# Kernel tuning notes

Hardware: AMD Instinct MI355X
Metric: run time of the kernel (lower is better)

Reference implementation:

```python
import jax, jax.numpy as jnp
import numpy as np
from jax import lax

B, CIN, H, W = 2, 512, 64, 64
CD = CIN // 2            # down_dim = 256
CQ = CD // 8             # q/k channels = 32
EPS = 1e-5               # BatchNorm eps


def _conv3(x, w, b):
    # 3x3 conv, stride 1, padding 1 (init padding=1), NCHW/OIHW
    y = lax.conv_general_dilated(x, w, (1, 1), [(1, 1), (1, 1)],
                                 dimension_numbers=('NCHW', 'OIHW', 'NCHW'))
    return y + b[None, :, None, None]


def _bn(x, g, b, m, v):
    scale = g / jnp.sqrt(v + EPS)
    return x * scale[None, :, None, None] + (b - m * scale)[None, :, None, None]


def _prelu(x, a):
    return jnp.where(x > 0, x, a * x)


def _p1(x, w, b):
    # 1x1 conv as channel matmul
    return jnp.einsum('bchw,oc->bohw', x, w) + b[None, :, None, None]


def setup_inputs() -> dict:
    key = jax.random.key(0)
    it = iter(jax.random.split(key, 64))
    def nrm(shape, s=0.05):
        return jax.random.normal(next(it), shape, jnp.float32) * s
    inp = {
        'input_rgb': jax.random.normal(next(it), (B, CIN, H, W), jnp.float32),
        'input_dsm': jax.random.normal(next(it), (B, CIN, H, W), jnp.float32),
    }
    for m in ('rgb', 'dsm'):
        inp['conv_w_' + m] = nrm((CD, CIN, 3, 3))
        inp['conv_b_' + m] = nrm((CD,))
        inp['bn_g_' + m] = 1.0 + nrm((CD,))
        inp['bn_b_' + m] = nrm((CD,))
        inp['bn_m_' + m] = nrm((CD,))
        inp['bn_v_' + m] = jax.random.uniform(next(it), (CD,), jnp.float32, 0.5, 1.5)
        inp['prelu_' + m] = jnp.float32(0.25)
        inp['q_w_' + m] = nrm((CQ, CD)); inp['q_b_' + m] = nrm((CQ,))
        inp['k_w_' + m] = nrm((CQ, CD)); inp['k_b_' + m] = nrm((CQ,))
        inp['v_w_' + m] = nrm((CD, CD)); inp['v_b_' + m] = nrm((CD,))
        inp['up_w_' + m] = nrm((CIN, CD)); inp['up_b_' + m] = nrm((CIN,))
        inp['gamma_' + m] = jnp.float32(0.1)  # learned residual gate (zero-init in torch)
    return inp


def reference(input_rgb, input_dsm,
              conv_w_rgb, conv_b_rgb, bn_g_rgb, bn_b_rgb, bn_m_rgb, bn_v_rgb, prelu_rgb,
              q_w_rgb, q_b_rgb, k_w_rgb, k_b_rgb, v_w_rgb, v_b_rgb, up_w_rgb, up_b_rgb, gamma_rgb,
              conv_w_dsm, conv_b_dsm, bn_g_dsm, bn_b_dsm, bn_m_dsm, bn_v_dsm, prelu_dsm,
              q_w_dsm, q_b_dsm, k_w_dsm, k_b_dsm, v_w_dsm, v_b_dsm, up_w_dsm, up_b_dsm, gamma_dsm):
    conv_rgb = _prelu(_bn(_conv3(input_rgb, conv_w_rgb, conv_b_rgb),
                          bn_g_rgb, bn_b_rgb, bn_m_rgb, bn_v_rgb), prelu_rgb)
    conv_dsm = _prelu(_bn(_conv3(input_dsm, conv_w_dsm, conv_b_dsm),
                          bn_g_dsm, bn_b_dsm, bn_m_dsm, bn_v_dsm), prelu_dsm)
    b, c, h, w = conv_rgb.shape
    n = h * w
    q_rgb = _p1(conv_rgb, q_w_rgb, q_b_rgb).reshape(b, CQ, n)
    k_rgb = _p1(conv_rgb, k_w_rgb, k_b_rgb).reshape(b, CQ, n)
    v_rgb = _p1(conv_rgb, v_w_rgb, v_b_rgb).reshape(b, c, n)
    q_dsm = _p1(conv_dsm, q_w_dsm, q_b_dsm).reshape(b, CQ, n)
    k_dsm = _p1(conv_dsm, k_w_dsm, k_b_dsm).reshape(b, CQ, n)
    v_dsm = _p1(conv_dsm, v_w_dsm, v_b_dsm).reshape(b, c, n)
    # cross-modal unscaled attention: dsm queries attend over rgb keys
    attn_rgb = jax.nn.softmax(jnp.einsum('bqn,bqm->bnm', q_dsm, k_rgb), axis=-1)  # [b,n,n]
    o_rgb = jnp.einsum('bcj,bij->bci', v_rgb, attn_rgb).reshape(b, c, h, w)
    o_rgb = gamma_rgb * o_rgb + conv_rgb
    attn_dsm = jax.nn.softmax(jnp.einsum('bqn,bqm->bnm', q_rgb, k_dsm), axis=-1)
    o_dsm = jnp.einsum('bcj,bij->bci', v_dsm, attn_dsm).reshape(b, c, h, w)
    o_dsm = gamma_dsm * o_dsm + conv_dsm
    out_rgb = _p1(o_rgb, up_w_rgb, up_b_rgb) + input_rgb
    out_dsm = _p1(o_dsm, up_w_dsm, up_b_dsm) + input_dsm
    return (out_rgb, out_dsm)
```

## Files before the change

### kernel.cpp

```cpp
#include <hip/hip_runtime.h>
#include <hip/hip_bf16.h>
#include <stdint.h>


constexpr int CINCH = 512;
constexpr int NPIX  = 4096;

typedef __bf16 bf16x8 __attribute__((ext_vector_type(8)));
typedef __bf16 bf16x4 __attribute__((ext_vector_type(4)));
typedef float  f32x4  __attribute__((ext_vector_type(4)));

__device__ __forceinline__ __bf16 f2b(float f) {
    __hip_bfloat16 h = __float2bfloat16(f);
    return *reinterpret_cast<__bf16*>(&h);
}

__device__ __forceinline__ void load_lds16(const void* g, void* l) {
    __builtin_amdgcn_global_load_lds(
        (const __attribute__((address_space(1))) unsigned int*)(uintptr_t)g,
        (__attribute__((address_space(3))) unsigned int*)(uintptr_t)l,
        16, 0, 0);
}

__global__ __launch_bounds__(256)
void prep_w(const float* __restrict__ w_r, const float* __restrict__ w_d,
            const float* __restrict__ cb_r, const float* __restrict__ bg_r,
            const float* __restrict__ bb_r, const float* __restrict__ bm_r,
            const float* __restrict__ bv_r,
            const float* __restrict__ cb_d, const float* __restrict__ bg_d,
            const float* __restrict__ bb_d, const float* __restrict__ bm_d,
            const float* __restrict__ bv_d,
            __bf16* __restrict__ Wt, float* __restrict__ scA,
            float* __restrict__ shB, __bf16* __restrict__ zrow)
{
    const int t = threadIdx.x;
    const int blk = blockIdx.x;
    if (blk < 2304) {
        int gid = blk * 1024 + t * 4;
        int mod = gid >= 1179648;
        int o2  = gid - mod * 1179648;
        int tap = o2 >> 17;
        int r   = o2 & 131071;
        int oc  = r >> 9;
        int ic  = r & 511;
        const float* wsrc = mod ? w_d : w_r;
        long base = ((long)(oc * 512 + ic)) * 9 + tap;
        bf16x4 v;
        v.x = f2b(wsrc[base]);
        v.y = f2b(wsrc[base + 9]);
        v.z = f2b(wsrc[base + 18]);
        v.w = f2b(wsrc[base + 27]);
        *(bf16x4*)&Wt[gid] = v;
    } else if (blk == 2304) {
        unsigned short* z = (unsigned short*)zrow;
        z[t] = 0; z[t + 256] = 0;
    } else {
        int mod = blk - 2305;
        const float* cb = mod ? cb_d : cb_r;
        const float* bg = mod ? bg_d : bg_r;
        const float* bb = mod ? bb_d : bb_r;
        const float* bm = mod ? bm_d : bm_r;
        const float* bv = mod ? bv_d : bv_r;
        int oc = t;
        float sc = bg[oc] * rsqrtf(bv[oc] + 1e-5f);
        scA[mod * 256 + oc] = sc;
        shB[mod * 256 + oc] = (cb[oc] - bm[oc]) * sc + bb[oc];
    }
}

__global__ __launch_bounds__(256)
void prep_gw(const float* __restrict__ qw_r, const float* __restrict__ qw_d,
             const float* __restrict__ kw_r, const float* __restrict__ kw_d,
             const float* __restrict__ vw_r, const float* __restrict__ vw_d,
             const float* __restrict__ uw_r, const float* __restrict__ uw_d,
             __bf16* __restrict__ Wq, __bf16* __restrict__ Wk,
             __bf16* __restrict__ Wv, __bf16* __restrict__ Wu)
{
    int gid = blockIdx.x * 1024 + threadIdx.x * 4;
    __bf16* dst;
    float4 f = make_float4(0.f, 0.f, 0.f, 0.f);
    if (gid < 65536) {
        int mod = gid >> 15, e = gid & 32767;
        dst = Wq + gid;
        if (e < 8192) f = *(const float4*)((mod ? qw_d : qw_r) + e);
    } else if (gid < 131072) {
        int g = gid - 65536;
        int mod = g >> 15, e = g & 32767;
        dst = Wk + g;
        if (e < 8192) f = *(const float4*)((mod ? kw_d : kw_r) + e);
    } else if (gid < 262144) {
        int g = gid - 131072;
        int mod = g >> 16, e = g & 65535;
        dst = Wv + g;
        f = *(const float4*)((mod ? vw_d : vw_r) + e);
    } else {
        int g = gid - 262144;
        int mod = g >> 17, e = g & 131071;
        dst = Wu + g;
        f = *(const float4*)((mod ? uw_d : uw_r) + e);
    }
    bf16x4 o; o.x = f2b(f.x); o.y = f2b(f.y); o.z = f2b(f.z); o.w = f2b(f.w);
    *(bf16x4*)dst = o;
}

__global__ __launch_bounds__(256)
void xpose(const float* __restrict__ inr, const float* __restrict__ ind,
           __bf16* __restrict__ Xp)
{
    __shared__ float tile[32][33];
    const int t = threadIdx.x;
    const int p0 = blockIdx.x * 32;
    const int ic0 = blockIdx.y * 32;
    const int mb = blockIdx.z;
    const int mod = mb >> 1, b = mb & 1;
    const float* src = (mod ? ind : inr) + (long)b * CINCH * NPIX;

    int i = t >> 3, j4 = (t & 7) * 4;
    float4 v = *(const float4*)&src[(long)(ic0 + i) * NPIX + p0 + j4];
    tile[i][j4 + 0] = v.x; tile[i][j4 + 1] = v.y;
    tile[i][j4 + 2] = v.z; tile[i][j4 + 3] = v.w;
    __syncthreads();
    int j = t >> 3, i4 = (t & 7) * 4;
    bf16x4 o;
    o.x = f2b(tile[i4 + 0][j]);
    o.y = f2b(tile[i4 + 1][j]);
    o.z = f2b(tile[i4 + 2][j]);
    o.w = f2b(tile[i4 + 3][j]);
    *(bf16x4*)&Xp[((long)mb * NPIX + p0 + j) * 512 + ic0 + i4] = o;
}

__global__ __launch_bounds__(256)
void t256(const float* __restrict__ src, __bf16* __restrict__ dst)
{
    __shared__ float tile[32][33];
    const int t = threadIdx.x;
    const int p0 = blockIdx.x * 32;
    const int c0 = blockIdx.y * 32;
    const int mb = blockIdx.z;
    const float* s = src + (long)mb * 256 * NPIX;
    __bf16* d = dst + (long)mb * NPIX * 256;

    int i = t >> 3, j4 = (t & 7) * 4;
    float4 v = *(const float4*)&s[(long)(c0 + i) * NPIX + p0 + j4];
    tile[i][j4 + 0] = v.x; tile[i][j4 + 1] = v.y;
    tile[i][j4 + 2] = v.z; tile[i][j4 + 3] = v.w;
    __syncthreads();
    int j = t >> 3, i4 = (t & 7) * 4;
    bf16x4 o;
    o.x = f2b(tile[i4 + 0][j]); o.y = f2b(tile[i4 + 1][j]);
    o.z = f2b(tile[i4 + 2][j]); o.w = f2b(tile[i4 + 3][j]);
    *(bf16x4*)&d[((long)(p0 + j)) * 256 + c0 + i4] = o;
}

__global__ __launch_bounds__(256)
void conv_mfma(const __bf16* __restrict__ Wt, const __bf16* __restrict__ Xp,
               const __bf16* __restrict__ zrow, const float* __restrict__ scA,
               const float* __restrict__ shB, const float* __restrict__ prr,
               const float* __restrict__ prd, float* __restrict__ conv)
{
    __shared__ __bf16 As[3 * 64 * 64];
    __shared__ __bf16 Bs[2 * 385 * 64];

    const int t = threadIdx.x;
    const int y0 = blockIdx.x * 4;
    const int m0 = blockIdx.y * 64;
    const int mb = blockIdx.z;
    const int mod = mb >> 1;

    const __bf16* Am = Wt + (long)mod * (9 * 256 * 512);
    const __bf16* Xb = Xp + (long)mb * NPIX * 512;

    const int lane = t & 63, quad = lane >> 4, l15 = lane & 15, w = t >> 6;

    if (t < 16)
        *(f32x4*)((char*)Bs + (t >> 3) * 49280 + 49152 + (t & 7) * 16) = (f32x4)0.f;
    asm volatile("s_waitcnt lgkmcnt(0)" ::: "memory");

    auto stage_a = [&](int buf, int tap, int cc) {
#pragma unroll
        for (int k = 0; k < 2; ++k) {
            int r  = w * 16 + k * 8 + (lane >> 3);
            int sl = (lane & 7) ^ (r & 7);
            const __bf16* src = Am + (long)tap * 131072 + (long)(m0 + r) * 512
                              + cc * 64 + sl * 8;
            load_lds16(src, (char*)As + buf * 8192 + (w * 16 + k * 8) * 128);
        }
    };
    auto stage_b = [&](int buf, int cc) {
#pragma unroll
        for (int k = 0; k < 12; ++k) {
            int r  = w * 96 + k * 8 + (lane >> 3);
            int sl = (lane & 7) ^ (r & 7);
            int hr = r >> 6, xx = r & 63;
            int gy = y0 + hr - 1;
            const __bf16* src = ((unsigned)gy < 64u)
                ? Xb + (long)(gy * 64 + xx) * 512 + cc * 64 + sl * 8
                : zrow + sl * 8;
            load_lds16(src, (char*)Bs + buf * 49280 + (w * 96 + k * 8) * 128);
        }
    };

    f32x4 acc[4][4];
#pragma unroll
    for (int i = 0; i < 4; ++i)
#pragma unroll
        for (int j = 0; j < 4; ++j) acc[i][j] = (f32x4)0.f;

    stage_b(0, 0);
    stage_a(0, 0, 0);
    stage_a(1, 1, 0);

    const int soffA0 = ((quad ^ (l15 & 7)) << 4);
    const int soffA1 = (((4 | quad) ^ (l15 & 7)) << 4);

    for (int c = 0; c < 8; ++c) {
        for (int tp = 0; tp < 9; ++tp) {
            const int s = c * 9 + tp;
            if (s == 71)                  { asm volatile("s_waitcnt vmcnt(0)" ::: "memory"); }
            else if (tp >= 7 && c < 7)    { asm volatile("s_waitcnt vmcnt(14)" ::: "memory"); }
            else                          { asm volatile("s_waitcnt vmcnt(2)" ::: "memory"); }
            __builtin_amdgcn_sched_barrier(0);
            __builtin_amdgcn_s_barrier();
            __builtin_amdgcn_sched_barrier(0);

            if (s + 2 < 72) {
                int c2 = (tp + 2 >= 9) ? c + 1 : c;
                int t2 = (tp + 2 >= 9) ? tp - 7 : tp + 2;
                int b2 = (s + 2) % 3;
                stage_a(b2, t2, c2);
            }
            __builtin_amdgcn_sched_barrier(0);
            if (tp == 6 && c < 7) stage_b((c + 1) & 1, c + 1);
            __builtin_amdgcn_sched_barrier(0);

            const char* ab = (const char*)As + (s % 3) * 8192;
            const char* bb = (const char*)Bs + (c & 1) * 49280;
            const int dy = tp / 3 - 1, dx = tp % 3 - 1;
            const int hr = w + 1 + dy;
            int rb[4];
#pragma unroll
            for (int fj = 0; fj < 4; ++fj) {
                int x = fj * 16 + l15 + dx;
                rb[fj] = ((unsigned)x < 64u) ? hr * 64 + x : 384;
            }
#pragma unroll
            for (int kk = 0; kk < 2; ++kk) {
                const int slq = kk * 4 + quad;
                bf16x8 af[4], bfr[4];
#pragma unroll
                for (int i = 0; i < 4; ++i)
                    af[i] = *(const bf16x8*)(ab + (16 * i + l15) * 128
                                             + (kk ? soffA1 : soffA0));
#pragma unroll
                for (int fj = 0; fj < 4; ++fj)
                    bfr[fj] = *(const bf16x8*)(bb + rb[fj] * 128
                                               + ((slq ^ (rb[fj] & 7)) << 4));
#pragma unroll
                for (int i = 0; i < 4; ++i)
#pragma unroll
                    for (int fj = 0; fj < 4; ++fj)
                        acc[i][fj] = __builtin_amdgcn_mfma_f32_16x16x32_bf16(
                            af[i], bfr[fj], acc[i][fj], 0, 0, 0);
            }
        }
    }

    const float alpha = (mod ? prd : prr)[0];
    float* outp = conv + (long)mb * 256 * NPIX;
    const int nbase = (y0 + w) * 64;
#pragma unroll
    for (int i = 0; i < 4; ++i) {
#pragma unroll
        for (int r = 0; r < 4; ++r) {
            int oc = m0 + 16 * i + quad * 4 + r;
            float sc = scA[mod * 256 + oc];
            float sh = shB[mod * 256 + oc];
            float* orow = outp + (long)oc * NPIX;
#pragma unroll
            for (int fj = 0; fj < 4; ++fj) {
                int n = nbase + 16 * fj + l15;
                float y = acc[i][fj][r] * sc + sh;
                y = (y > 0.f) ? y : alpha * y;
                orow[n] = y;
            }
        }
    }
}

__global__ __launch_bounds__(256)
void proj_mfma(const __bf16* __restrict__ Wb, int mstride,
               const __bf16* __restrict__ Bt,
               const float* __restrict__ bias_r, const float* __restrict__ bias_d,
               __bf16* __restrict__ dstT, __bf16* __restrict__ dstV,
               float* __restrict__ dstU,
               const float* __restrict__ resid_r, const float* __restrict__ resid_d,
               int mode, float oscale)
{
    __shared__ __bf16 As[128 * 32];
    __shared__ __bf16 Bs[128 * 32];

    const int t = threadIdx.x;
    const int n0 = blockIdx.x * 128;
    const int m0 = blockIdx.y * 128;
    const int mb = blockIdx.z;
    const int mod = mb >> 1, b = mb & 1;

    const __bf16* Am = Wb + (long)mod * mstride;
    const __bf16* Bm = Bt + (long)mb * (NPIX * 256);
    const float* bias = mod ? bias_d : bias_r;

    const int rowa = t >> 2, c16 = t & 3;
    char* ldsA0 = (char*)As + (t >> 6) * 1024;
    char* ldsA1 = ldsA0 + 4096;
    char* ldsB0 = (char*)Bs + (t >> 6) * 1024;
    char* ldsB1 = ldsB0 + 4096;
    const __bf16* srcA = Am + (long)(m0 + rowa) * 256 + c16 * 8;
    const __bf16* srcB = Bm + (long)(n0 + rowa) * 256 + c16 * 8;

    const int lane = t & 63, quad = lane >> 4, l15 = lane & 15, w = t >> 6;
    const int mw = (w >> 1) * 64, nw = (w & 1) * 64;
    const char* abase = (const char*)As + (mw + l15) * 64 + quad * 16;
    const char* bbase = (const char*)Bs + (nw + l15) * 64 + quad * 16;

    f32x4 acc[4][4];
#pragma unroll
    for (int i = 0; i < 4; ++i)
#pragma unroll
        for (int j = 0; j < 4; ++j) acc[i][j] = (f32x4)0.f;

    for (int kc = 0; kc < 256; kc += 32) {
        load_lds16(srcA + kc, ldsA0);
        load_lds16(srcA + kc + 16384, ldsA1);
        load_lds16(srcB + kc, ldsB0);
        load_lds16(srcB + kc + 16384, ldsB1);
        __syncthreads();

        bf16x8 af[4], bfr[4];
#pragma unroll
        for (int i = 0; i < 4; ++i) af[i]  = *(const bf16x8*)(abase + i * 1024);
#pragma unroll
        for (int j = 0; j < 4; ++j) bfr[j] = *(const bf16x8*)(bbase + j * 1024);
#pragma unroll
        for (int i = 0; i < 4; ++i)
#pragma unroll
            for (int j = 0; j < 4; ++j)
                acc[i][j] = __builtin_amdgcn_mfma_f32_16x16x32_bf16(
                    af[i], bfr[j], acc[i][j], 0, 0, 0);
        __syncthreads();
    }

    if (mode == 0) {
        if (mw == 0) {
            __bf16* dbase = dstT + (long)mb * (NPIX * 32);
#pragma unroll
            for (int fi = 0; fi < 2; ++fi)
#pragma unroll
                for (int r = 0; r < 4; ++r) {
                    int oc = 16 * fi + quad * 4 + r;
                    float bi = bias[oc];
#pragma unroll
                    for (int fj = 0; fj < 4; ++fj) {
                        int n = n0 + nw + 16 * fj + l15;
                        dbase[(long)n * 32 + oc] = f2b((acc[fi][fj][r] + bi) * oscale);
                    }
                }
        }
    } else if (mode == 1) {
        __bf16* dv = dstV + (long)mb * (256 * NPIX);
#pragma unroll
        for (int fi = 0; fi < 4; ++fi)
#pragma unroll
            for (int r = 0; r < 4; ++r) {
                int c = m0 + mw + 16 * fi + quad * 4 + r;
                float bi = bias[c];
                __bf16* row = dv + (long)c * NPIX;
#pragma unroll
                for (int fj = 0; fj < 4; ++fj) {
                    int n = n0 + nw + 16 * fj + l15;
                    row[n] = f2b(acc[fi][fj][r] + bi);
                }
            }
    } else {
        float* du = dstU + (long)mod * 4194304 + (long)b * 2097152;
        const float* rs = (mod ? resid_d : resid_r) + (long)b * 2097152;
#pragma unroll
        for (int fi = 0; fi < 4; ++fi)
#pragma unroll
            for (int r = 0; r < 4; ++r) {
                int oc = m0 + mw + 16 * fi + quad * 4 + r;
                float bi = bias[oc];
                const float* rrow = rs + (long)oc * NPIX;
                float* orow = du + (long)oc * NPIX;
#pragma unroll
                for (int fj = 0; fj < 4; ++fj) {
                    int n = n0 + nw + 16 * fj + l15;
                    orow[n] = acc[fi][fj][r] + bi + rrow[n];
                }
            }
    }
}

__global__ __launch_bounds__(256)
void attn_stats_mfma(const __bf16* __restrict__ Qt, const __bf16* __restrict__ Kt,
                     float* __restrict__ rmp, float* __restrict__ rlp)
{
    __shared__ __bf16 Qs[128 * 32];
    __shared__ __bf16 Ks[128 * 32];
    __shared__ float redm[2][128];
    __shared__ float redl[2][128];

    const int t  = threadIdx.x;
    const int i0 = blockIdx.x * 128;
    const int mbo = blockIdx.y;
    const int o  = mbo >> 1, b = mbo & 1;
    const int seg = blockIdx.z;
    const int jbase = seg * 1024;
    const int mbK = o * 2 + b, mbQ = (1 - o) * 2 + b;

    const __bf16* Qg = Qt + (long)mbQ * 131072;
    const __bf16* Kg = Kt + (long)mbK * 131072;

    const int lane = t & 63, quad = lane >> 4, l15 = lane & 15, w = t >> 6;
    const int mS = (w >> 1) * 64;
    const int nS = (w & 1) * 64;

    load_lds16((const char*)Qg + (long)i0 * 64 + t * 16, (char*)Qs + w * 1024);
    load_lds16((const char*)Qg + (long)i0 * 64 + 4096 + t * 16,
               (char*)Qs + 4096 + w * 1024);
    __syncthreads();

    bf16x8 qa[4];
#pragma unroll
    for (int fi = 0; fi < 4; ++fi)
        qa[fi] = *(const bf16x8*)((const char*)Qs + (mS + 16 * fi + l15) * 64 + quad * 16);

    const f32x4 zero4 = (f32x4)0.f;
    float m_t[16], l_t[16];
#pragma unroll
    for (int e = 0; e < 16; ++e) { m_t[e] = -3.0e38f; l_t[e] = 0.f; }

    for (int j0 = jbase; j0 < jbase + 1024; j0 += 128) {
        __syncthreads();
        load_lds16((const char*)Kg + (long)j0 * 64 + t * 16, (char*)Ks + w * 1024);
        load_lds16((const char*)Kg + (long)j0 * 64 + 4096 + t * 16,
                   (char*)Ks + 4096 + w * 1024);
        __syncthreads();

        bf16x8 kb[4];
#pragma unroll
        for (int fj = 0; fj < 4; ++fj)
            kb[fj] = *(const bf16x8*)((const char*)Ks + (nS + 16 * fj + l15) * 64 + quad * 16);
#pragma unroll
        for (int fi = 0; fi < 4; ++fi) {
            f32x4 sf[4];
#pragma unroll
            for (int fj = 0; fj < 4; ++fj)
                sf[fj] = __builtin_amdgcn_mfma_f32_16x16x32_bf16(qa[fi], kb[fj], zero4, 0, 0, 0);
#pragma unroll
            for (int r = 0; r < 4; ++r) {
                int e = fi * 4 + r;
                float a = fmaxf(fmaxf(sf[0][r], sf[1][r]), fmaxf(sf[2][r], sf[3][r]));
                float nm = fmaxf(m_t[e], a);
                float s = exp2f(sf[0][r] - nm) + exp2f(sf[1][r] - nm)
                        + exp2f(sf[2][r] - nm) + exp2f(sf[3][r] - nm);
                l_t[e] = l_t[e] * exp2f(m_t[e] - nm) + s;
                m_t[e] = nm;
            }
        }
    }

#pragma unroll
    for (int d = 1; d < 16; d <<= 1)
#pragma unroll
        for (int e = 0; e < 16; ++e) {
            float om = __shfl_xor(m_t[e], d, 64);
            float ol = __shfl_xor(l_t[e], d, 64);
            float nm = fmaxf(m_t[e], om);
            l_t[e] = l_t[e] * exp2f(m_t[e] - nm) + ol * exp2f(om - nm);
            m_t[e] = nm;
        }
    if (l15 == 0) {
#pragma unroll
        for (int fi = 0; fi < 4; ++fi)
#pragma unroll
            for (int r = 0; r < 4; ++r) {
                redm[w & 1][mS + 16 * fi + quad * 4 + r] = m_t[fi * 4 + r];
                redl[w & 1][mS + 16 * fi + quad * 4 + r] = l_t[fi * 4 + r];
            }
    }
    __syncthreads();
    if (t < 128) {
        float m0 = redm[0][t], m1 = redm[1][t];
        float l0 = redl[0][t], l1 = redl[1][t];
        float m = fmaxf(m0, m1);
        float l = l0 * exp2f(m0 - m) + l1 * exp2f(m1 - m);
        rmp[seg * 16384 + mbo * 4096 + i0 + t] = m;
        rlp[seg * 16384 + mbo * 4096 + i0 + t] = l;
    }
}

__global__ __launch_bounds__(256)
void stats_merge(const float* __restrict__ rmp, const float* __restrict__ rlp,
                 float* __restrict__ rmb, float* __restrict__ rlb)
{
    int idx = blockIdx.x * 256 + threadIdx.x;
    float m = rmp[idx];
#pragma unroll
    for (int s = 1; s < 4; ++s) m = fmaxf(m, rmp[s * 16384 + idx]);
    float l = 0.f;
#pragma unroll
    for (int s = 0; s < 4; ++s)
        l += rlp[s * 16384 + idx] * exp2f(rmp[s * 16384 + idx] - m);
    rmb[idx] = m;
    rlb[idx] = 1.f / l;
}

__global__ __launch_bounds__(256)
void attn_pv_mfma(const __bf16* __restrict__ Qt, const __bf16* __restrict__ Kt,
                  const __bf16* __restrict__ Vb,
                  float* __restrict__ part0, float* __restrict__ part1,
                  const float* __restrict__ rmb, const float* __restrict__ rlb)
{
    __shared__ __bf16 Qs[64 * 32];
    __shared__ __bf16 Ks[64 * 32];
    __shared__ __bf16 Vs[2 * 256 * 32];
    __shared__ __bf16 Ps[64 * 64];

    const int t  = threadIdx.x;
    const int i0 = blockIdx.x * 64;
    const int seg = blockIdx.y;
    const int mb = blockIdx.z;
    const int o  = mb >> 1, b = mb & 1;
    const int mbK = mb, mbQ = (1 - o) * 2 + b;
    const int jbase = seg * 2048;

    const __bf16* Qg = Qt + (long)mbQ * 131072;
    const __bf16* Kg = Kt + (long)mbK * 131072;
    const __bf16* Vg = Vb + (long)mbK * 1048576;
    const float* rm = rmb + mb * 4096;
    const float* rl = rlb + mb * 4096;

    const int lane = t & 63, quad = lane >> 4, l15 = lane & 15, w = t >> 6;
    const int iS = w * 16;
    const int cw = w * 64;

    load_lds16((const char*)Qg + (long)i0 * 64 + t * 16, (char*)Qs + w * 1024);

    float mlv[4], rlv[4];
#pragma unroll
    for (int r = 0; r < 4; ++r) mlv[r] = rm[i0 + iS + quad * 4 + r];
#pragma unroll
    for (int fj = 0; fj < 4; ++fj) rlv[fj] = rl[i0 + 16 * fj + l15];

    f32x4 acc[4][4];
#pragma unroll
    for (int i = 0; i < 4; ++i)
#pragma unroll
        for (int j = 0; j < 4; ++j) acc[i][j] = (f32x4)0.f;
    const f32x4 zero4 = (f32x4)0.f;

    __syncthreads();
    const bf16x8 qa = *(const bf16x8*)((const char*)Qs + (iS + l15) * 64 + quad * 16);

    const int clv = w * 16 + (lane >> 2);
    const int jb8 = (lane & 3) * 8;

    for (int j0 = jbase; j0 < jbase + 2048; j0 += 64) {
        __syncthreads();
        load_lds16((const char*)Kg + (long)j0 * 64 + t * 16, (char*)Ks + w * 1024);
        __syncthreads();

#pragma unroll
        for (int ii = 0; ii < 8; ++ii) {
            int ks = ii >> 2;
            int c = (ii & 3) * 64 + clv;
            load_lds16((const char*)Vg + (long)c * 8192 + (long)(j0 + ks * 32 + jb8) * 2,
                       (char*)Vs + ii * 4096 + w * 1024);
        }

        f32x4 sA[4];
#pragma unroll
        for (int fj = 0; fj < 4; ++fj) {
            bf16x8 kb = *(const bf16x8*)((const char*)Ks + (16 * fj + l15) * 64 + quad * 16);
            sA[fj] = __builtin_amdgcn_mfma_f32_16x16x32_bf16(qa, kb, zero4, 0, 0, 0);
        }
#pragma unroll
        for (int fj = 0; fj < 4; ++fj)
#pragma unroll
            for (int r = 0; r < 4; ++r) {
                int il = iS + quad * 4 + r;
                int boff = (il * 128 + (16 * fj + l15) * 2) ^ ((il & 12) << 3);
                *(__bf16*)((char*)Ps + boff) = f2b(exp2f(sA[fj][r] - mlv[r]));
            }
        __syncthreads();

#pragma unroll
        for (int ks = 0; ks < 2; ++ks) {
            bf16x8 va[4], pb[4];
#pragma unroll
            for (int fi = 0; fi < 4; ++fi)
                va[fi] = *(const bf16x8*)((const char*)Vs + ks * 16384 +
                                          (cw + 16 * fi + l15) * 64 + quad * 16);
#pragma unroll
            for (int fj = 0; fj < 4; ++fj) {
                int ip = 16 * fj + l15;
                int boff = (ip * 128 + ks * 64 + quad * 16) ^ ((ip & 12) << 3);
                pb[fj] = *(const bf16x8*)((const char*)Ps + boff);
            }
#pragma unroll
            for (int fi = 0; fi < 4; ++fi)
#pragma unroll
                for (int fj = 0; fj < 4; ++fj)
                    acc[fi][fj] = __builtin_amdgcn_mfma_f32_16x16x32_bf16(
                        va[fi], pb[fj], acc[fi][fj], 0, 0, 0);
        }
    }

    float* pg = (seg ? part1 : part0) + (long)mb * 1048576;
#pragma unroll
    for (int fi = 0; fi < 4; ++fi) {
#pragma unroll
        for (int r = 0; r < 4; ++r) {
            int c = cw + 16 * fi + quad * 4 + r;
            float* zr = pg + (long)c * 4096;
#pragma unroll
            for (int fj = 0; fj < 4; ++fj)
                zr[i0 + 16 * fj + l15] = acc[fi][fj][r] * rlv[fj];
        }
    }
}

__global__ __launch_bounds__(256)
void zred_t(const float* __restrict__ p0, const float* __restrict__ p1,
            const float* __restrict__ convb, __bf16* __restrict__ Zt,
            const float* __restrict__ g_r, const float* __restrict__ g_d)
{
    __shared__ float tile[32][33];
    const int t = threadIdx.x;
    const int pix0 = blockIdx.x * 32;
    const int c0 = blockIdx.y * 32;
    const int mb = blockIdx.z;
    const int o = mb >> 1;
    const float gamma = (o ? g_d : g_r)[0];
    const long base = (long)mb * 1048576;

    int i = t >> 3, j4 = (t & 7) * 4;
    long row = base + (long)(c0 + i) * 4096 + pix0 + j4;
    float4 a = *(const float4*)&p0[row];
    float4 b = *(const float4*)&p1[row];
    float4 cv = *(const float4*)&convb[row];
    tile[i][j4 + 0] = gamma * (a.x + b.x) + cv.x;
    tile[i][j4 + 1] = gamma * (a.y + b.y) + cv.y;
    tile[i][j4 + 2] = gamma * (a.z + b.z) + cv.z;
    tile[i][j4 + 3] = gamma * (a.w + b.w) + cv.w;
    __syncthreads();
    int j = t >> 3, i4 = (t & 7) * 4;
    bf16x4 oq;
    oq.x = f2b(tile[i4 + 0][j]); oq.y = f2b(tile[i4 + 1][j]);
    oq.z = f2b(tile[i4 + 2][j]); oq.w = f2b(tile[i4 + 3][j]);
    *(bf16x4*)&Zt[(long)mb * NPIX * 256 + (long)(pix0 + j) * 256 + c0 + i4] = oq;
}

extern "C" void kernel_launch(void* const* d_in, const int* in_sizes, int n_in,
                              void* d_out, int out_size, void* d_ws, size_t ws_size,
                              hipStream_t stream)
{
    const float* in_rgb = (const float*)d_in[0];
    const float* in_dsm = (const float*)d_in[1];
    auto P = [&](int i) { return (const float*)d_in[i]; };

    float* ws    = (float*)d_ws;
    float* conv  = ws;
    float* part0 = ws + 4194304;
    float* rmb   = ws + 8388608;
    float* rlb   = ws + 8404992;
    float* rmp   = part0;
    float* rlp   = part0 + 65536;
    float* scA   = ws + 8486912;
    float* shB   = ws + 8487424;
    __bf16* zrow = (__bf16*)(ws + 8487936);
    __bf16* Wt   = (__bf16*)(ws + 8488192);
    __bf16* Xp   = (__bf16*)(ws + 9667840);
    float*  part1 = ws + 9667840;
    __bf16* Qt   = (__bf16*)(ws + 13862144);
    __bf16* Kt   = (__bf16*)(ws + 14124288);
    __bf16* Vbb  = (__bf16*)(ws + 14386432);
    __bf16* Ct   = (__bf16*)(ws + 16483584);
    __bf16* Zt   = (__bf16*)(ws + 18580736);
    __bf16* Wq   = (__bf16*)(ws + 20677888);
    __bf16* Wk   = (__bf16*)(ws + 20710656);
    __bf16* Wv   = (__bf16*)(ws + 20743424);
    __bf16* Wu   = (__bf16*)(ws + 20808960);

    prep_w<<<2307, 256, 0, stream>>>(
        P(2), P(18), P(3), P(4), P(5), P(6), P(7),
        P(19), P(20), P(21), P(22), P(23),
        Wt, scA, shB, zrow);
    prep_gw<<<512, 256, 0, stream>>>(
        P(9), P(25), P(11), P(27), P(13), P(29), P(15), P(31),
        Wq, Wk, Wv, Wu);
    xpose<<<dim3(128, 16, 4), 256, 0, stream>>>(in_rgb, in_dsm, Xp);

    conv_mfma<<<dim3(16, 4, 4), 256, 0, stream>>>(
        Wt, Xp, zrow, scA, shB, P(8), P(24), conv);
    t256<<<dim3(128, 8, 4), 256, 0, stream>>>(conv, Ct);

    proj_mfma<<<dim3(32, 1, 4), 256, 0, stream>>>(
        Wq, 32768, Ct, P(10), P(26), Qt, nullptr, nullptr, nullptr, nullptr,
        0, 1.4426950408889634f);
    proj_mfma<<<dim3(32, 1, 4), 256, 0, stream>>>(
        Wk, 32768, Ct, P(12), P(28), Kt, nullptr, nullptr, nullptr, nullptr,
        0, 1.0f);
    proj_mfma<<<dim3(32, 2, 4), 256, 0, stream>>>(
        Wv, 65536, Ct, P(14), P(30), nullptr, Vbb, nullptr, nullptr, nullptr,
        1, 1.0f);

    attn_stats_mfma<<<dim3(32, 4, 4), 256, 0, stream>>>(Qt, Kt, rmp, rlp);
    stats_merge<<<64, 256, 0, stream>>>(rmp, rlp, rmb, rlb);

    attn_pv_mfma<<<dim3(64, 2, 4), 256, 0, stream>>>(
        Qt, Kt, Vbb, part0, part1, rmb, rlb);

    zred_t<<<dim3(128, 8, 4), 256, 0, stream>>>(
        part0, part1, conv, Zt, P(17), P(33));

    proj_mfma<<<dim3(32, 4, 4), 256, 0, stream>>>(
        Wu, 131072, Zt, P(16), P(32), nullptr, nullptr, (float*)d_out,
        in_rgb, in_dsm, 2, 1.0f);
}
```

Baseline: 367.0 us.

## Triple-buffer K/V loads, double P tile, and swizzle LDS in attention kernels

The PV attention kernel now handles 128 query rows per block instead of 64. K and V tiles are triple-buffered in LDS and the next stage is issued before computing the current one, with manual waitcnt and raw barriers in place of __syncthreads. The P tile is double-buffered, and both the stats and PV kernels use an XOR swizzle on global-to-LDS load offsets to reduce bank conflicts. The grid is flattened so that blocks sharing a K/V head are interleaved, aiming at L2 reuse. The cost is much larger LDS use and 128 accumulator registers, which forces one block per CU.

```diff
diff --git a/kernel.cpp b/kernel.cpp
--- a/kernel.cpp
+++ b/kernel.cpp
@@ -424,15 +424,19 @@
     const int mS = (w >> 1) * 64;
     const int nS = (w & 1) * 64;
 
-    load_lds16((const char*)Qg + (long)i0 * 64 + t * 16, (char*)Qs + w * 1024);
-    load_lds16((const char*)Qg + (long)i0 * 64 + 4096 + t * 16,
+    const int drow = w * 16 + (lane >> 2);
+    const int ssl  = ((lane & 3) ^ ((lane >> 3) & 3)) * 16;
+    const int rsl  = (quad ^ ((l15 >> 1) & 3)) << 4;
+
+    load_lds16((const char*)Qg + (long)(i0 + drow) * 64 + ssl, (char*)Qs + w * 1024);
+    load_lds16((const char*)Qg + (long)(i0 + 64 + drow) * 64 + ssl,
                (char*)Qs + 4096 + w * 1024);
     __syncthreads();
 
     bf16x8 qa[4];
 #pragma unroll
     for (int fi = 0; fi < 4; ++fi)
-        qa[fi] = *(const bf16x8*)((const char*)Qs + (mS + 16 * fi + l15) * 64 + quad * 16);
+        qa[fi] = *(const bf16x8*)((const char*)Qs + (mS + 16 * fi + l15) * 64 + rsl);
 
     const f32x4 zero4 = (f32x4)0.f;
     float m_t[16], l_t[16];
@@ -441,15 +445,15 @@
 
     for (int j0 = jbase; j0 < jbase + 1024; j0 += 128) {
         __syncthreads();
-        load_lds16((const char*)Kg + (long)j0 * 64 + t * 16, (char*)Ks + w * 1024);
-        load_lds16((const char*)Kg + (long)j0 * 64 + 4096 + t * 16,
+        load_lds16((const char*)Kg + (long)(j0 + drow) * 64 + ssl, (char*)Ks + w * 1024);
+        load_lds16((const char*)Kg + (long)(j0 + 64 + drow) * 64 + ssl,
                    (char*)Ks + 4096 + w * 1024);
         __syncthreads();
 
         bf16x8 kb[4];
 #pragma unroll
         for (int fj = 0; fj < 4; ++fj)
-            kb[fj] = *(const bf16x8*)((const char*)Ks + (nS + 16 * fj + l15) * 64 + quad * 16);
+            kb[fj] = *(const bf16x8*)((const char*)Ks + (nS + 16 * fj + l15) * 64 + rsl);
 #pragma unroll
         for (int fi = 0; fi < 4; ++fi) {
             f32x4 sf[4];
@@ -515,102 +519,136 @@
     rlb[idx] = 1.f / l;
 }
 
-__global__ __launch_bounds__(256)
+__global__ __launch_bounds__(256, 1)
 void attn_pv_mfma(const __bf16* __restrict__ Qt, const __bf16* __restrict__ Kt,
                   const __bf16* __restrict__ Vb,
                   float* __restrict__ part0, float* __restrict__ part1,
                   const float* __restrict__ rmb, const float* __restrict__ rlb)
 {
-    __shared__ __bf16 Qs[64 * 32];
-    __shared__ __bf16 Ks[64 * 32];
-    __shared__ __bf16 Vs[2 * 256 * 32];
-    __shared__ __bf16 Ps[64 * 64];
+    __shared__ __bf16 Qs[128 * 32];
+    __shared__ __bf16 Ks[3 * 64 * 32];
+    __shared__ __bf16 Vs[3 * 2 * 256 * 32];
+    __shared__ __bf16 Ps[2 * 128 * 64];
 
     const int t  = threadIdx.x;
-    const int i0 = blockIdx.x * 64;
-    const int seg = blockIdx.y;
-    const int mb = blockIdx.z;
+    const int bx = blockIdx.x;
+    const int grp = bx & 7;
+    const int i0  = (bx >> 3) * 128;
+    const int seg = grp & 1;
+    const int mb  = grp >> 1;
     const int o  = mb >> 1, b = mb & 1;
-    const int mbK = mb, mbQ = (1 - o) * 2 + b;
+    const int mbQ = (1 - o) * 2 + b;
     const int jbase = seg * 2048;
 
     const __bf16* Qg = Qt + (long)mbQ * 131072;
-    const __bf16* Kg = Kt + (long)mbK * 131072;
-    const __bf16* Vg = Vb + (long)mbK * 1048576;
+    const __bf16* Kg = Kt + (long)mb * 131072;
+    const __bf16* Vg = Vb + (long)mb * 1048576;
     const float* rm = rmb + mb * 4096;
     const float* rl = rlb + mb * 4096;
 
     const int lane = t & 63, quad = lane >> 4, l15 = lane & 15, w = t >> 6;
-    const int iS = w * 16;
+    const int iw = w * 32;
     const int cw = w * 64;
 
-    load_lds16((const char*)Qg + (long)i0 * 64 + t * 16, (char*)Qs + w * 1024);
-
-    float mlv[4], rlv[4];
-#pragma unroll
-    for (int r = 0; r < 4; ++r) mlv[r] = rm[i0 + iS + quad * 4 + r];
-#pragma unroll
-    for (int fj = 0; fj < 4; ++fj) rlv[fj] = rl[i0 + 16 * fj + l15];
-
-    f32x4 acc[4][4];
-#pragma unroll
-    for (int i = 0; i < 4; ++i)
-#pragma unroll
-        for (int j = 0; j < 4; ++j) acc[i][j] = (f32x4)0.f;
-    const f32x4 zero4 = (f32x4)0.f;
-
-    __syncthreads();
-    const bf16x8 qa = *(const bf16x8*)((const char*)Qs + (iS + l15) * 64 + quad * 16);
-
-    const int clv = w * 16 + (lane >> 2);
-    const int jb8 = (lane & 3) * 8;
-
-    for (int j0 = jbase; j0 < jbase + 2048; j0 += 64) {
-        __syncthreads();
-        load_lds16((const char*)Kg + (long)j0 * 64 + t * 16, (char*)Ks + w * 1024);
-        __syncthreads();
-
+    const int drow = w * 16 + (lane >> 2);
+    const int ssl  = ((lane & 3) ^ ((lane >> 3) & 3)) * 16;
+    const int rsl  = (quad ^ ((l15 >> 1) & 3)) << 4;
+
+    float mlv[8], rlv[8];
+#pragma unroll
+    for (int fi = 0; fi < 2; ++fi)
+#pragma unroll
+        for (int r = 0; r < 4; ++r)
+            mlv[fi * 4 + r] = rm[i0 + iw + 16 * fi + quad * 4 + r];
+#pragma unroll
+    for (int fj = 0; fj < 8; ++fj) rlv[fj] = rl[i0 + 16 * fj + l15];
+    asm volatile("s_waitcnt vmcnt(0)" ::: "memory");
+
+    load_lds16((const char*)Qg + (long)(i0 + drow) * 64 + ssl, (char*)Qs + w * 1024);
+    load_lds16((const char*)Qg + (long)(i0 + 64 + drow) * 64 + ssl,
+               (char*)Qs + 4096 + w * 1024);
+    asm volatile("s_waitcnt vmcnt(0)" ::: "memory");
+    __builtin_amdgcn_s_barrier();
+    bf16x8 qa[2];
+    qa[0] = *(const bf16x8*)((const char*)Qs + (iw + l15) * 64 + rsl);
+    qa[1] = *(const bf16x8*)((const char*)Qs + (iw + 16 + l15) * 64 + rsl);
+
+    auto stage = [&](int sidx) {
+        const int buf = sidx % 3;
+        const int j0 = jbase + sidx * 64;
+        load_lds16((const char*)Kg + (long)(j0 + drow) * 64 + ssl,
+                   (char*)Ks + buf * 4096 + w * 1024);
 #pragma unroll
         for (int ii = 0; ii < 8; ++ii) {
             int ks = ii >> 2;
-            int c = (ii & 3) * 64 + clv;
-            load_lds16((const char*)Vg + (long)c * 8192 + (long)(j0 + ks * 32 + jb8) * 2,
-                       (char*)Vs + ii * 4096 + w * 1024);
-        }
-
-        f32x4 sA[4];
+            int c  = (ii & 3) * 64 + drow;
+            load_lds16((const char*)Vg + (long)c * 8192 + (long)(j0 + ks * 32) * 2 + ssl,
+                       (char*)Vs + buf * 32768 + ii * 4096 + w * 1024);
+        }
+    };
+
+    f32x4 acc[4][8];
+#pragma unroll
+    for (int i = 0; i < 4; ++i)
+#pragma unroll
+        for (int j = 0; j < 8; ++j) acc[i][j] = (f32x4)0.f;
+    const f32x4 zero4 = (f32x4)0.f;
+
+    stage(0);
+
+    for (int s = 0; s < 32; ++s) {
+        if (s + 1 < 32) {
+            stage(s + 1);
+            asm volatile("s_waitcnt vmcnt(9)" ::: "memory");
+        } else {
+            asm volatile("s_waitcnt vmcnt(0)" ::: "memory");
+        }
+        __builtin_amdgcn_sched_barrier(0);
+        __builtin_amdgcn_s_barrier();
+        __builtin_amdgcn_sched_barrier(0);
+
+        const char* kbp = (const char*)Ks + (s % 3) * 4096;
+        f32x4 sA[2][4];
 #pragma unroll
         for (int fj = 0; fj < 4; ++fj) {
-            bf16x8 kb = *(const bf16x8*)((const char*)Ks + (16 * fj + l15) * 64 + quad * 16);
-            sA[fj] = __builtin_amdgcn_mfma_f32_16x16x32_bf16(qa, kb, zero4, 0, 0, 0);
-        }
-#pragma unroll
-        for (int fj = 0; fj < 4; ++fj)
-#pragma unroll
-            for (int r = 0; r < 4; ++r) {
-                int il = iS + quad * 4 + r;
-                int boff = (il * 128 + (16 * fj + l15) * 2) ^ ((il & 12) << 3);
-                *(__bf16*)((char*)Ps + boff) = f2b(exp2f(sA[fj][r] - mlv[r]));
-            }
-        __syncthreads();
-
+            bf16x8 kb = *(const bf16x8*)(kbp + (16 * fj + l15) * 64 + rsl);
+            sA[0][fj] = __builtin_amdgcn_mfma_f32_16x16x32_bf16(qa[0], kb, zero4, 0, 0, 0);
+            sA[1][fj] = __builtin_amdgcn_mfma_f32_16x16x32_bf16(qa[1], kb, zero4, 0, 0, 0);
+        }
+        char* pst = (char*)Ps + (s & 1) * 16384;
+#pragma unroll
+        for (int fi = 0; fi < 2; ++fi)
+#pragma unroll
+            for (int fj = 0; fj < 4; ++fj)
+#pragma unroll
+                for (int r = 0; r < 4; ++r) {
+                    int il = iw + 16 * fi + quad * 4 + r;
+                    int boff = (il * 128 + (16 * fj + l15) * 2) ^ ((il & 7) << 4);
+                    *(__bf16*)(pst + boff) = f2b(exp2f(sA[fi][fj][r] - mlv[fi * 4 + r]));
+                }
+        __builtin_amdgcn_sched_barrier(0);
+        __builtin_amdgcn_s_barrier();
+        __builtin_amdgcn_sched_barrier(0);
+
+        const char* vbp = (const char*)Vs + (s % 3) * 32768;
+        const char* prd = (const char*)Ps + (s & 1) * 16384;
 #pragma unroll
         for (int ks = 0; ks < 2; ++ks) {
-            bf16x8 va[4], pb[4];
+            bf16x8 va[4], pb[8];
 #pragma unroll
             for (int fi = 0; fi < 4; ++fi)
-                va[fi] = *(const bf16x8*)((const char*)Vs + ks * 16384 +
-                                          (cw + 16 * fi + l15) * 64 + quad * 16);
-#pragma unroll
-            for (int fj = 0; fj < 4; ++fj) {
+                va[fi] = *(const bf16x8*)(vbp + ks * 16384 +
+                                          (cw + 16 * fi + l15) * 64 + rsl);
+#pragma unroll
+            for (int fj = 0; fj < 8; ++fj) {
                 int ip = 16 * fj + l15;
-                int boff = (ip * 128 + ks * 64 + quad * 16) ^ ((ip & 12) << 3);
-                pb[fj] = *(const bf16x8*)((const char*)Ps + boff);
+                int boff = (ip * 128 + ks * 64 + quad * 16) ^ ((ip & 7) << 4);
+                pb[fj] = *(const bf16x8*)(prd + boff);
             }
 #pragma unroll
             for (int fi = 0; fi < 4; ++fi)
 #pragma unroll
-                for (int fj = 0; fj < 4; ++fj)
+                for (int fj = 0; fj < 8; ++fj)
                     acc[fi][fj] = __builtin_amdgcn_mfma_f32_16x16x32_bf16(
                         va[fi], pb[fj], acc[fi][fj], 0, 0, 0);
         }
@@ -624,7 +662,7 @@
             int c = cw + 16 * fi + quad * 4 + r;
             float* zr = pg + (long)c * 4096;
 #pragma unroll
-            for (int fj = 0; fj < 4; ++fj)
+            for (int fj = 0; fj < 8; ++fj)
                 zr[i0 + 16 * fj + l15] = acc[fi][fj][r] * rlv[fj];
         }
     }
@@ -718,7 +756,7 @@
     attn_stats_mfma<<<dim3(32, 4, 4), 256, 0, stream>>>(Qt, Kt, rmp, rlp);
     stats_merge<<<64, 256, 0, stream>>>(rmp, rlp, rmb, rlb);
 
-    attn_pv_mfma<<<dim3(64, 2, 4), 256, 0, stream>>>(
+    attn_pv_mfma<<<256, 256, 0, stream>>>(
         Qt, Kt, Vbb, part0, part1, rmb, rlb);
 
     zred_t<<<dim3(128, 8, 4), 256, 0, stream>>>(
```

Result: no change. 374.0 us (+1.9%).

## Swizzle LDS layouts for Q/K/V tiles and remap attention PV block order

Applied to the files above, without the earlier changes.

Changes the global-to-LDS load mapping for Q, K and V tiles in the attention stats and PV kernels to an XOR-swizzled layout, with matching swizzled reads, to reduce LDS bank conflicts on the MFMA operand loads. The Ps tile swizzle pattern is also changed. The PV kernel switches to a 1D grid where adjacent blocks share the same query tile across modality/segment, which may change cache locality. A launch-bounds occupancy hint of 2 blocks per SIMD set is added, which may constrain register allocation.

```diff
diff --git a/kernel.cpp b/kernel.cpp
--- a/kernel.cpp
+++ b/kernel.cpp
@@ -424,15 +424,19 @@
     const int mS = (w >> 1) * 64;
     const int nS = (w & 1) * 64;
 
-    load_lds16((const char*)Qg + (long)i0 * 64 + t * 16, (char*)Qs + w * 1024);
-    load_lds16((const char*)Qg + (long)i0 * 64 + 4096 + t * 16,
+    const int drow = w * 16 + (lane >> 2);
+    const int ssl  = ((lane & 3) ^ ((lane >> 3) & 3)) * 16;
+    const int rsl  = (quad ^ ((l15 >> 1) & 3)) << 4;
+
+    load_lds16((const char*)Qg + (long)(i0 + drow) * 64 + ssl, (char*)Qs + w * 1024);
+    load_lds16((const char*)Qg + (long)(i0 + 64 + drow) * 64 + ssl,
                (char*)Qs + 4096 + w * 1024);
     __syncthreads();
 
     bf16x8 qa[4];
 #pragma unroll
     for (int fi = 0; fi < 4; ++fi)
-        qa[fi] = *(const bf16x8*)((const char*)Qs + (mS + 16 * fi + l15) * 64 + quad * 16);
+        qa[fi] = *(const bf16x8*)((const char*)Qs + (mS + 16 * fi + l15) * 64 + rsl);
 
     const f32x4 zero4 = (f32x4)0.f;
     float m_t[16], l_t[16];
@@ -441,15 +445,15 @@
 
     for (int j0 = jbase; j0 < jbase + 1024; j0 += 128) {
         __syncthreads();
-        load_lds16((const char*)Kg + (long)j0 * 64 + t * 16, (char*)Ks + w * 1024);
-        load_lds16((const char*)Kg + (long)j0 * 64 + 4096 + t * 16,
+        load_lds16((const char*)Kg + (long)(j0 + drow) * 64 + ssl, (char*)Ks + w * 1024);
+        load_lds16((const char*)Kg + (long)(j0 + 64 + drow) * 64 + ssl,
                    (char*)Ks + 4096 + w * 1024);
         __syncthreads();
 
         bf16x8 kb[4];
 #pragma unroll
         for (int fj = 0; fj < 4; ++fj)
-            kb[fj] = *(const bf16x8*)((const char*)Ks + (nS + 16 * fj + l15) * 64 + quad * 16);
+            kb[fj] = *(const bf16x8*)((const char*)Ks + (nS + 16 * fj + l15) * 64 + rsl);
 #pragma unroll
         for (int fi = 0; fi < 4; ++fi) {
             f32x4 sf[4];
@@ -515,7 +519,7 @@
     rlb[idx] = 1.f / l;
 }
 
-__global__ __launch_bounds__(256)
+__global__ __launch_bounds__(256, 2)
 void attn_pv_mfma(const __bf16* __restrict__ Qt, const __bf16* __restrict__ Kt,
                   const __bf16* __restrict__ Vb,
                   float* __restrict__ part0, float* __restrict__ part1,
@@ -527,16 +531,18 @@
     __shared__ __bf16 Ps[64 * 64];
 
     const int t  = threadIdx.x;
-    const int i0 = blockIdx.x * 64;
-    const int seg = blockIdx.y;
-    const int mb = blockIdx.z;
+    const int bx = blockIdx.x;
+    const int grp = bx & 7;
+    const int i0  = (bx >> 3) * 64;
+    const int seg = grp & 1;
+    const int mb  = grp >> 1;
     const int o  = mb >> 1, b = mb & 1;
-    const int mbK = mb, mbQ = (1 - o) * 2 + b;
+    const int mbQ = (1 - o) * 2 + b;
     const int jbase = seg * 2048;
 
     const __bf16* Qg = Qt + (long)mbQ * 131072;
-    const __bf16* Kg = Kt + (long)mbK * 131072;
-    const __bf16* Vg = Vb + (long)mbK * 1048576;
+    const __bf16* Kg = Kt + (long)mb * 131072;
+    const __bf16* Vg = Vb + (long)mb * 1048576;
     const float* rm = rmb + mb * 4096;
     const float* rl = rlb + mb * 4096;
 
@@ -544,7 +550,11 @@
     const int iS = w * 16;
     const int cw = w * 64;
 
-    load_lds16((const char*)Qg + (long)i0 * 64 + t * 16, (char*)Qs + w * 1024);
+    const int drow = w * 16 + (lane >> 2);
+    const int ssl  = ((lane & 3) ^ ((lane >> 3) & 3)) * 16;
+    const int rsl  = (quad ^ ((l15 >> 1) & 3)) << 4;
+
+    load_lds16((const char*)Qg + (long)(i0 + drow) * 64 + ssl, (char*)Qs + w * 1024);
 
     float mlv[4], rlv[4];
 #pragma unroll
@@ -560,28 +570,26 @@
     const f32x4 zero4 = (f32x4)0.f;
 
     __syncthreads();
-    const bf16x8 qa = *(const bf16x8*)((const char*)Qs + (iS + l15) * 64 + quad * 16);
-
-    const int clv = w * 16 + (lane >> 2);
-    const int jb8 = (lane & 3) * 8;
+    const bf16x8 qa = *(const bf16x8*)((const char*)Qs + (iS + l15) * 64 + rsl);
 
     for (int j0 = jbase; j0 < jbase + 2048; j0 += 64) {
         __syncthreads();
-        load_lds16((const char*)Kg + (long)j0 * 64 + t * 16, (char*)Ks + w * 1024);
+        load_lds16((const char*)Kg + (long)(j0 + drow) * 64 + ssl,
+                   (char*)Ks + w * 1024);
         __syncthreads();
 
 #pragma unroll
         for (int ii = 0; ii < 8; ++ii) {
             int ks = ii >> 2;
-            int c = (ii & 3) * 64 + clv;
-            load_lds16((const char*)Vg + (long)c * 8192 + (long)(j0 + ks * 32 + jb8) * 2,
+            int c  = (ii & 3) * 64 + drow;
+            load_lds16((const char*)Vg + (long)c * 8192 + (long)(j0 + ks * 32) * 2 + ssl,
                        (char*)Vs + ii * 4096 + w * 1024);
         }
 
         f32x4 sA[4];
 #pragma unroll
         for (int fj = 0; fj < 4; ++fj) {
-            bf16x8 kb = *(const bf16x8*)((const char*)Ks + (16 * fj + l15) * 64 + quad * 16);
+            bf16x8 kb = *(const bf16x8*)((const char*)Ks + (16 * fj + l15) * 64 + rsl);
             sA[fj] = __builtin_amdgcn_mfma_f32_16x16x32_bf16(qa, kb, zero4, 0, 0, 0);
         }
 #pragma unroll
@@ -589,7 +597,7 @@
 #pragma unroll
             for (int r = 0; r < 4; ++r) {
                 int il = iS + quad * 4 + r;
-                int boff = (il * 128 + (16 * fj + l15) * 2) ^ ((il & 12) << 3);
+                int boff = (il * 128 + (16 * fj + l15) * 2) ^ ((il & 7) << 4);
                 *(__bf16*)((char*)Ps + boff) = f2b(exp2f(sA[fj][r] - mlv[r]));
             }
         __syncthreads();
@@ -600,11 +608,11 @@
 #pragma unroll
             for (int fi = 0; fi < 4; ++fi)
                 va[fi] = *(const bf16x8*)((const char*)Vs + ks * 16384 +
-                                          (cw + 16 * fi + l15) * 64 + quad * 16);
+                                          (cw + 16 * fi + l15) * 64 + rsl);
 #pragma unroll
             for (int fj = 0; fj < 4; ++fj) {
                 int ip = 16 * fj + l15;
-                int boff = (ip * 128 + ks * 64 + quad * 16) ^ ((ip & 12) << 3);
+                int boff = (ip * 128 + ks * 64 + quad * 16) ^ ((ip & 7) << 4);
                 pb[fj] = *(const bf16x8*)((const char*)Ps + boff);
             }
 #pragma unroll
@@ -718,7 +726,7 @@
     attn_stats_mfma<<<dim3(32, 4, 4), 256, 0, stream>>>(Qt, Kt, rmp, rlp);
     stats_merge<<<64, 256, 0, stream>>>(rmp, rlp, rmb, rlb);
 
-    attn_pv_mfma<<<dim3(64, 2, 4), 256, 0, stream>>>(
+    attn_pv_mfma<<<512, 256, 0, stream>>>(
         Qt, Kt, Vbb, part0, part1, rmb, rlb);
 
     zred_t<<<dim3(128, 8, 4), 256, 0, stream>>>(
```

After: 363.5 us. Within noise of the previous version (-1.0%).
